# Kernel optimization log

Hardware: AMD Instinct MI355X
Metric: run time of the kernel (lower is better)

The kernel has to match this reference:

```python
import jax, jax.numpy as jnp
import numpy as np

BN_EPS = 1e-6
LN_EPS = 1e-5
ROPE_BASE = 10000.0


def rope(x):
    # x: [..., S, d] ; standard half-split rotary embedding, positions 0..S-1
    S, d = x.shape[-2], x.shape[-1]
    half = d // 2
    inv_freq = 1.0 / (ROPE_BASE ** (jnp.arange(half, dtype=jnp.float32) / half))
    ang = jnp.arange(S, dtype=jnp.float32)[:, None] * inv_freq[None, :]  # [S, half]
    cos, sin = jnp.cos(ang), jnp.sin(ang)
    x1, x2 = x[..., :half], x[..., half:]
    return jnp.concatenate([x1 * cos - x2 * sin, x1 * sin + x2 * cos], axis=-1)


def layernorm(x, g, b):
    m = jnp.mean(x, axis=-1, keepdims=True)
    v = jnp.mean((x - m) ** 2, axis=-1, keepdims=True)
    return (x - m) * jax.lax.rsqrt(v + LN_EPS) * g + b


def rms_batchnorm(x, g, b, running):
    # eval-mode RMSBatchNorm1D: normalize by running RMS^2 buffer
    return x * jax.lax.rsqrt(running + BN_EPS) * g + b


def setup_inputs() -> dict:
    B, S, C, H, QD, KD, VD = 4, 2048, 1536, 8, 128, 128, 192
    key = jax.random.key(0)
    ks = jax.random.split(key, 8)
    sc = 0.02
    return {
        'x': jax.random.normal(ks[0], (B, S, C), dtype=jnp.float32),
        'rms_g': jnp.ones((C,), jnp.float32),
        'rms_b': jnp.zeros((C,), jnp.float32),
        'rms_r': jnp.ones((C,), jnp.float32),
        'Wq': jax.random.normal(ks[1], (H * QD, C), jnp.float32) * sc,
        'Wk': jax.random.normal(ks[2], (KD, C), jnp.float32) * sc,
        'Wv': jax.random.normal(ks[3], (VD, C), jnp.float32) * sc,
        'q_g': jnp.ones((QD,), jnp.float32), 'q_b': jnp.zeros((QD,), jnp.float32),
        'k_g': jnp.ones((KD,), jnp.float32), 'k_b': jnp.zeros((KD,), jnp.float32),
        'v_g': jnp.ones((VD,), jnp.float32), 'v_b': jnp.zeros((VD,), jnp.float32),
        'Wo': jax.random.normal(ks[4], (C, H * VD), jnp.float32) * sc,
        'bo': jnp.zeros((C,), jnp.float32),
        'on_g': jnp.ones((C,), jnp.float32),
        'on_b': jnp.zeros((C,), jnp.float32),
        'on_r': jnp.ones((C,), jnp.float32),
    }


def reference(x, rms_g, rms_b, rms_r, Wq, Wk, Wv, q_g, q_b, k_g, k_b, v_g, v_b, Wo, bo, on_g, on_b, on_r):
    B, S, C = x.shape
    H, QD = 8, Wq.shape[0] // 8
    KD, VD = Wk.shape[0], Wv.shape[0]

    xn = rms_batchnorm(x, rms_g, rms_b, rms_r)

    q = (xn @ Wq.T).reshape(B, S, H, QD)       # [B,S,H,QD]
    q = layernorm(q, q_g, q_b)
    k = layernorm(xn @ Wk.T, k_g, k_b)          # [B,S,KD] shared across heads (MQA)
    v = layernorm(xn @ Wv.T, v_g, v_b)          # [B,S,VD]

    # RoPE along sequence dim
    q = rope(jnp.transpose(q, (0, 2, 1, 3)))    # [B,H,S,QD]
    k = rope(k)
    v = rope(v)

    scale = 1.0 / jnp.sqrt(jnp.float32(KD))
    logits = jnp.einsum('bhsc,bSc->bhsS', q, k) * scale   # [B,H,S,S]
    attn = jax.nn.softmax(logits, axis=-1)
    o = jnp.einsum('bhsS,bSc->bshc', attn, v).reshape(B, S, H * VD)

    y = o @ Wo.T + bo                            # [B,S,C]
    y = rms_batchnorm(y, on_g, on_b, on_r)
    # dropout is identity in eval mode
    return y
```

## Files before the change

kernel.cpp:

```cpp
#include <hip/hip_runtime.h>
#include <math.h>

typedef unsigned short u16;
typedef unsigned int   u32;
typedef __attribute__((ext_vector_type(8))) short bf16x8;
typedef __attribute__((ext_vector_type(4))) float f32x4;

#define DEVI static __device__ __forceinline__

constexpr int Bb = 4, Ss = 2048, Cc = 1536, Hh = 8, QD = 128, KD = 128, VD = 192;
constexpr int NTOK = Bb * Ss;
constexpr int NQKV = Hh*QD + KD + VD;
constexpr int NQKV_PAD = 1536;
constexpr float ATTN_SCALE = 0.08838834764831845f;

constexpr size_t OFF_S1  = 0;
constexpr size_t OFF_B1  = OFF_S1 + Cc*4;
constexpr size_t OFF_S2  = OFF_B1 + Cc*4;
constexpr size_t OFF_B2  = OFF_S2 + Cc*4;
constexpr size_t OFF_CT  = 24576;
constexpr size_t OFF_ST  = OFF_CT  + (size_t)Ss*64*4;
constexpr size_t OFF_CTV = OFF_ST  + (size_t)Ss*64*4;
constexpr size_t OFF_STV = OFF_CTV + (size_t)Ss*96*4;
constexpr size_t OFF_WQKV= OFF_STV + (size_t)Ss*96*4;
constexpr size_t OFF_WO  = OFF_WQKV+ (size_t)NQKV_PAD*Cc*2;
constexpr size_t OFF_XN  = OFF_WO  + (size_t)Cc*Cc*2;
constexpr size_t OFF_QKV = OFF_XN  + (size_t)NTOK*Cc*2;
constexpr size_t OFF_Q   = OFF_QKV + (size_t)NTOK*NQKV*2;
constexpr size_t OFF_K   = OFF_Q   + (size_t)NTOK*(Hh*QD)*2;
constexpr size_t OFF_VT  = OFF_K   + (size_t)NTOK*KD*2;

DEVI u16 f2b(float f) {
  union { float f; u32 u; } v; v.f = f;
  u32 r = v.u + 0x7FFFu + ((v.u >> 16) & 1u);
  return (u16)(r >> 16);
}
DEVI float b2f(u16 h) {
  union { u32 u; float f; } v; v.u = ((u32)h) << 16;
  return v.f;
}
DEVI u32 cvtpk(float lo, float hi) {
  u32 r;
  asm("v_cvt_pk_bf16_f32 %0, %1, %2" : "=v"(r) : "v"(lo), "v"(hi));
  return r;
}
DEVI void gload16(const void* g, void* l) {
  __builtin_amdgcn_global_load_lds(g, l, 16, 0, 0);
}
DEVI f32x4 mfma16(bf16x8 a, bf16x8 b, f32x4 c) {
  return __builtin_amdgcn_mfma_f32_16x16x32_bf16(a, b, c, 0, 0, 0);
}
DEVI int swz64(int byte) {
  return byte ^ ((((byte>>7)&1)<<4) | (((byte>>8)&1)<<5));
}

__global__ __launch_bounds__(256) void k_prep_small(
    const float* __restrict__ rms_g, const float* __restrict__ rms_b, const float* __restrict__ rms_r,
    const float* __restrict__ on_g,  const float* __restrict__ on_b,  const float* __restrict__ on_r,
    const float* __restrict__ bo, char* __restrict__ ws)
{
  int i = blockIdx.x * 256 + threadIdx.x;
  float* s1 = (float*)(ws + OFF_S1);
  float* b1 = (float*)(ws + OFF_B1);
  float* s2 = (float*)(ws + OFF_S2);
  float* b2 = (float*)(ws + OFF_B2);
  float* ct = (float*)(ws + OFF_CT);
  float* st = (float*)(ws + OFF_ST);
  float* ctv= (float*)(ws + OFF_CTV);
  float* stv= (float*)(ws + OFF_STV);
  if (i < Cc) {
    float a = rsqrtf(rms_r[i] + 1e-6f) * rms_g[i];
    s1[i] = a; b1[i] = rms_b[i];
    float c = rsqrtf(on_r[i] + 1e-6f) * on_g[i];
    s2[i] = c; b2[i] = bo[i]*c + on_b[i];
  }
  int j = i - Cc;
  if (j >= 0 && j < Ss*64) {
    int s = j >> 6, f = j & 63;
    float invf = expf(-(float)f * (9.210340371976184f / 64.f));
    float ang = (float)s * invf;
    float sn, cs; sincosf(ang, &sn, &cs);
    ct[j] = cs; st[j] = sn;
  }
  int k = j - Ss*64;
  if (k >= 0 && k < Ss*96) {
    int s = k / 96, f = k - s*96;
    float invf = expf(-(float)f * (9.210340371976184f / 96.f));
    float ang = (float)s * invf;
    float sn, cs; sincosf(ang, &sn, &cs);
    ctv[k] = cs; stv[k] = sn;
  }
}

__global__ __launch_bounds__(256) void k_prep_w(
    const float* __restrict__ Wq, const float* __restrict__ Wk, const float* __restrict__ Wv,
    const float* __restrict__ Wo, char* __restrict__ ws)
{
  u16* wqkv = (u16*)(ws + OFF_WQKV);
  u16* wo   = (u16*)(ws + OFF_WO);
  const int total1 = NQKV_PAD * Cc;
  const int total2 = Cc * Cc;
  for (int i = blockIdx.x*256 + threadIdx.x; i < total1 + total2; i += gridDim.x*256) {
    if (i < total1) {
      int r = i / Cc, c = i - r*Cc;
      float v = 0.f;
      if (r < 1024)      v = Wq[(size_t)r*Cc + c];
      else if (r < 1152) v = Wk[(size_t)(r-1024)*Cc + c];
      else if (r < 1344) v = Wv[(size_t)(r-1152)*Cc + c];
      wqkv[i] = f2b(v);
    } else {
      int t2 = i - total1;
      wo[t2] = f2b(Wo[t2]);
    }
  }
}

__global__ __launch_bounds__(256) void k_xn(const float* __restrict__ x, char* __restrict__ ws)
{
  const float* s1 = (const float*)(ws + OFF_S1);
  const float* b1 = (const float*)(ws + OFF_B1);
  u16* xn = (u16*)(ws + OFF_XN);
  int idx = blockIdx.x*256 + threadIdx.x;
  float4 xv = ((const float4*)x)[idx];
  int c = (idx % (Cc/4)) * 4;
  u32 lo = (u32)f2b(xv.x*s1[c]   + b1[c])   | ((u32)f2b(xv.y*s1[c+1] + b1[c+1]) << 16);
  u32 hi = (u32)f2b(xv.z*s1[c+2] + b1[c+2]) | ((u32)f2b(xv.w*s1[c+3] + b1[c+3]) << 16);
  ((uint2*)xn)[idx] = make_uint2(lo, hi);
}

template <bool EPI>
__global__ __launch_bounds__(512, 2) void k_gemm256(
    const u16* __restrict__ A, const u16* __restrict__ Bw, void* __restrict__ outp,
    int K, int N_store, const float* __restrict__ s2, const float* __restrict__ b2)
{
  __shared__ u16 tiles[4][2][8192];
  const int tid = threadIdx.x;
  const int wid = tid >> 6, l = tid & 63;
  const int lr = l & 15, lh = l >> 4;
  const int wr = wid >> 2, wc = wid & 3;
  const int id  = blockIdx.x + gridDim.x * blockIdx.y;
  const int cpx = (gridDim.x * gridDim.y) >> 3;
  const int sw  = (id & 7) * cpx + (id >> 3);
  const int by  = sw / gridDim.x;
  const int bx  = sw - by * gridDim.x;
  const int m0 = by * 256, n0 = bx * 256;

  const size_t Kb = (size_t)K * 2;
  const char* aBase = (const char*)(A  + (size_t)m0 * K);
  const char* bBase = (const char*)(Bw + (size_t)n0 * K);
  const int o0    = wid*1024 + l*16;
  const int sfl   = swz64(o0);
  const size_t srowb = (size_t)(sfl >> 6) * Kb;
  const int scolb = sfl & 63;
  int aoff[8], boff[4];
#pragma unroll
  for (int mi = 0; mi < 8; mi++) aoff[mi] = swz64((wr*128 + mi*16 + lr)*64 + lh*16);
#pragma unroll
  for (int ni = 0; ni < 4; ni++) boff[ni] = swz64((wc*64  + ni*16 + lr)*64 + lh*16);

  f32x4 acc[8][4] = {};
  const int NT = K >> 5;

#define STAGE(t) {                                                        \
    char* la_ = (char*)tiles[(t) & 3][0] + wid*1024;                      \
    char* lb_ = (char*)tiles[(t) & 3][1] + wid*1024;                      \
    const char* ga_ = aBase + srowb + (size_t)(t)*64 + scolb;             \
    const char* gb_ = bBase + srowb + (size_t)(t)*64 + scolb;             \
    gload16(ga_,            la_);                                         \
    gload16(ga_ + 128*Kb,   la_ + 8192);                                  \
    gload16(gb_,            lb_);                                         \
    gload16(gb_ + 128*Kb,   lb_ + 8192);                                  \
  }

  STAGE(0); STAGE(1); STAGE(2);
  for (int t = 0; t < NT; ++t) {
    if (t + 3 < NT) STAGE(t + 3);
    asm volatile("s_waitcnt vmcnt(12)" ::: "memory");
    __builtin_amdgcn_s_barrier();
    const char* la = (const char*)tiles[t & 3][0];
    const char* lb = (const char*)tiles[t & 3][1];
    bf16x8 af[8], bfr[4];
#pragma unroll
    for (int mi = 0; mi < 8; mi++) af[mi]  = *(const bf16x8*)(la + aoff[mi]);
#pragma unroll
    for (int ni = 0; ni < 4; ni++) bfr[ni] = *(const bf16x8*)(lb + boff[ni]);
    __builtin_amdgcn_s_setprio(1);
#pragma unroll
    for (int mi = 0; mi < 8; mi++)
#pragma unroll
      for (int ni = 0; ni < 4; ni++)
        acc[mi][ni] = mfma16(af[mi], bfr[ni], acc[mi][ni]);
    __builtin_amdgcn_s_setprio(0);
    asm volatile("s_waitcnt lgkmcnt(0)" ::: "memory");
    __builtin_amdgcn_s_barrier();
  }
#undef STAGE

  const int r0 = m0 + wr*128 + lh*4;
  const int c0 = n0 + wc*64 + lr;
#pragma unroll
  for (int mi = 0; mi < 8; mi++) {
#pragma unroll
    for (int ni = 0; ni < 4; ni++) {
      int col = c0 + ni*16;
      if (col < N_store) {
#pragma unroll
        for (int r = 0; r < 4; r++) {
          size_t o = (size_t)(r0 + mi*16 + r) * N_store + col;
          if (EPI) ((float*)outp)[o] = acc[mi][ni][r] * s2[col] + b2[col];
          else     ((u16*)outp)[o]   = f2b(acc[mi][ni][r]);
        }
      }
    }
  }
}

__global__ __launch_bounds__(256) void k_lnrope_qk(
    char* __restrict__ ws,
    const float* __restrict__ q_g, const float* __restrict__ q_b,
    const float* __restrict__ k_g, const float* __restrict__ k_b)
{
  const u16* qkv = (const u16*)(ws + OFF_QKV);
  u16* qo = (u16*)(ws + OFF_Q);
  u16* ko = (u16*)(ws + OFF_K);
  const float* ct = (const float*)(ws + OFF_CT);
  const float* st = (const float*)(ws + OFF_ST);
  const int w = threadIdx.x >> 6, l = threadIdx.x & 63;
  const int rid = blockIdx.x*4 + w;
  const u16* src; u16* dst; const float* g; const float* bb; float osc; int s;
  if (rid < NTOK*Hh) {
    int t = rid >> 3, h = rid & 7;
    s = t & (Ss-1); int b = t >> 11;
    src = qkv + (size_t)t*NQKV + h*QD;
    dst = qo + ((size_t)(b*Hh + h)*Ss + s)*QD;
    g = q_g; bb = q_b; osc = ATTN_SCALE;
  } else {
    int t = rid - NTOK*Hh;
    s = t & (Ss-1);
    src = qkv + (size_t)t*NQKV + Hh*QD;
    dst = ko + (size_t)t*KD;
    g = k_g; bb = k_b; osc = 1.f;
  }
  u32 pk = *(const u32*)(src + 2*l);
  float x0 = b2f((u16)(pk & 0xFFFFu)), x1 = b2f((u16)(pk >> 16));
  float sm = x0 + x1, sq = x0*x0 + x1*x1;
#pragma unroll
  for (int off = 1; off < 64; off <<= 1) { sm += __shfl_xor(sm, off); sq += __shfl_xor(sq, off); }
  float mean = sm * (1.f/128.f);
  float var  = sq * (1.f/128.f) - mean*mean;
  float rstd = rsqrtf(var + 1e-5f);
  int d0 = 2*l;
  float y0 = (x0 - mean)*rstd*g[d0]   + bb[d0];
  float y1 = (x1 - mean)*rstd*g[d0+1] + bb[d0+1];
  float z0 = __shfl_xor(y0, 32);
  float z1 = __shfl_xor(y1, 32);
  int f0 = 2*(l & 31);
  float c0 = ct[s*64 + f0],     s0 = st[s*64 + f0];
  float c1 = ct[s*64 + f0 + 1], s1 = st[s*64 + f0 + 1];
  float o0, o1;
  if (l < 32) { o0 = y0*c0 - z0*s0; o1 = y1*c1 - z1*s1; }
  else        { o0 = z0*s0 + y0*c0; o1 = z1*s1 + y1*c1; }
  o0 *= osc; o1 *= osc;
  *(u32*)(dst + 2*l) = (u32)f2b(o0) | ((u32)f2b(o1) << 16);
}

__global__ __launch_bounds__(256) void k_lnrope_v(
    char* __restrict__ ws, const float* __restrict__ v_g, const float* __restrict__ v_b)
{
  const u16* qkv = (const u16*)(ws + OFF_QKV);
  u16* vo = (u16*)(ws + OFF_VT);
  const float* ct = (const float*)(ws + OFF_CTV);
  const float* st = (const float*)(ws + OFF_STV);
  __shared__ float buf[4][192];
  const int w = threadIdx.x >> 6, l = threadIdx.x & 63;
  const int t = blockIdx.x*4 + w;
  const int s = t & (Ss-1), b = t >> 11;
  const u16* src = qkv + (size_t)t*NQKV + Hh*QD + KD;
  float xs[3]; float sm = 0.f, sq = 0.f;
#pragma unroll
  for (int i2 = 0; i2 < 3; i2++) {
    float xv = b2f(src[l + 64*i2]);
    xs[i2] = xv; buf[w][l + 64*i2] = xv;
    sm += xv; sq += xv*xv;
  }
  __threadfence_block();
#pragma unroll
  for (int off = 1; off < 64; off <<= 1) { sm += __shfl_xor(sm, off); sq += __shfl_xor(sq, off); }
  float mean = sm * (1.f/192.f);
  float var  = sq * (1.f/192.f) - mean*mean;
  float rstd = rsqrtf(var + 1e-5f);
#pragma unroll
  for (int i2 = 0; i2 < 3; i2++) {
    int e = l + 64*i2;
    float val;
    if (e < 96) {
      float x1 = xs[i2], x2 = buf[w][e+96];
      float x1n = (x1-mean)*rstd*v_g[e]    + v_b[e];
      float x2n = (x2-mean)*rstd*v_g[e+96] + v_b[e+96];
      float cs = ct[s*96 + e], sn = st[s*96 + e];
      val = x1n*cs - x2n*sn;
    } else {
      int f = e - 96;
      float x2 = xs[i2], x1 = buf[w][f];
      float x1n = (x1-mean)*rstd*v_g[f] + v_b[f];
      float x2n = (x2-mean)*rstd*v_g[e] + v_b[e];
      float cs = ct[s*96 + f], sn = st[s*96 + f];
      val = x1n*sn + x2n*cs;
    }
    vo[((size_t)b*VD + e)*Ss + s] = f2b(val);
  }
}

__global__ __launch_bounds__(256, 2) void k_attn(const char* __restrict__ ws, u16* __restrict__ O)
{
  const u16* qs = (const u16*)(ws + OFF_Q);
  const u16* ks = (const u16*)(ws + OFF_K);
  const u16* vt = (const u16*)(ws + OFF_VT);
  __shared__ u16 k_lds[64*128];
  __shared__ u16 v_lds[192*64];
  __shared__ u16 p_lds[4][32][64];
  const int tid = threadIdx.x, w = tid >> 6, l = tid & 63;
  const int lr = l & 15, lh = l >> 4;
  const int bid0 = blockIdx.x;
  const int sw = (bid0 & 7)*64 + (bid0 >> 3);
  const int qt = sw & 15, h = (sw >> 4) & 7, b = sw >> 7;
  const int q0 = qt*128 + w*32;
  bf16x8 aq[2][4];
  const u16* qbase = qs + ((size_t)(b*Hh + h)*Ss + q0 + lr)*QD + lh*8;
#pragma unroll
  for (int h2 = 0; h2 < 2; h2++)
#pragma unroll
    for (int kk = 0; kk < 4; kk++)
      aq[h2][kk] = *(const bf16x8*)(qbase + (size_t)h2*16*QD + kk*32);
  float m[2] = {-INFINITY, -INFINITY}, sume[2] = {0.f, 0.f};
  f32x4 acc[2][12] = {};
  const char* ksrc0 = (const char*)(ks + (size_t)b*Ss*KD);
  const char* vsrc0 = (const char*)(vt + (size_t)b*VD*Ss);
  for (int kv0 = 0; kv0 < Ss; kv0 += 64) {
    {
      const char* ksrc = ksrc0 + (size_t)kv0*KD*2;
#pragma unroll
      for (int r = 0; r < 4; r++) {
        int o = r*4096 + w*1024 + l*16;
        gload16(ksrc + (o ^ (((o>>8)&7)<<4)), (char*)k_lds + r*4096 + w*1024);
      }
#pragma unroll
      for (int r = 0; r < 6; r++) {
        int o = r*4096 + w*1024 + l*16;
        int vd = o >> 7, c = o & 127;
        gload16(vsrc0 + (size_t)vd*(Ss*2) + kv0*2 + (c ^ ((vd&7)<<4)),
                (char*)v_lds + r*4096 + w*1024);
      }
    }
    __syncthreads();
    f32x4 sv[2][4] = {};
#pragma unroll
    for (int nt = 0; nt < 4; nt++) {
#pragma unroll
      for (int kk = 0; kk < 4; kk++) {
        int kb = ((nt*16 + lr) << 8) + kk*64 + lh*16;
        kb ^= (lr & 7) << 4;
        bf16x8 bk = *(const bf16x8*)((const char*)k_lds + kb);
        sv[0][nt] = mfma16(bk, aq[0][kk], sv[0][nt]);
        sv[1][nt] = mfma16(bk, aq[1][kk], sv[1][nt]);
      }
    }
#pragma unroll
    for (int h2 = 0; h2 < 2; h2++) {
      float tmx = -INFINITY;
#pragma unroll
      for (int nt = 0; nt < 4; nt++)
        tmx = fmaxf(tmx, fmaxf(fmaxf(sv[h2][nt][0], sv[h2][nt][1]),
                               fmaxf(sv[h2][nt][2], sv[h2][nt][3])));
      tmx = fmaxf(tmx, __shfl_xor(tmx, 16));
      tmx = fmaxf(tmx, __shfl_xor(tmx, 32));
      if (!__all(tmx - m[h2] <= 8.f)) {
        float mnew = fmaxf(m[h2], tmx);
        float scl = __expf(m[h2] - mnew);
        m[h2] = mnew; sume[h2] *= scl;
#pragma unroll
        for (int n = 0; n < 12; n++) acc[h2][n] *= scl;
      }
      float tsum = 0.f;
#pragma unroll
      for (int nt = 0; nt < 4; nt++) {
#pragma unroll
        for (int r2 = 0; r2 < 4; r2++) {
          float e = __expf(sv[h2][nt][r2] - m[h2]);
          sv[h2][nt][r2] = e; tsum += e;
        }
      }
      tsum += __shfl_xor(tsum, 16);
      tsum += __shfl_xor(tsum, 32);
      sume[h2] += tsum;
      {
        char* pw = (char*)&p_lds[w][h2*16 + lr][0];
#pragma unroll
        for (int nt = 0; nt < 4; nt++) {
          u32 w0 = cvtpk(sv[h2][nt][0], sv[h2][nt][1]);
          u32 w1 = cvtpk(sv[h2][nt][2], sv[h2][nt][3]);
          int pcol = (nt*32 + lh*8) ^ ((lr & 7) << 4);
          *(u32*)(pw + pcol)     = w0;
          *(u32*)(pw + pcol + 4) = w1;
        }
      }
    }
    asm volatile("s_waitcnt lgkmcnt(0)" ::: "memory");
    __builtin_amdgcn_sched_barrier(0);
#pragma unroll
    for (int kk2 = 0; kk2 < 2; kk2++) {
      int rcol = (kk2*64 + lh*16) ^ ((lr & 7) << 4);
      bf16x8 pb0 = *(const bf16x8*)((const char*)&p_lds[w][lr][0]      + rcol);
      bf16x8 pb1 = *(const bf16x8*)((const char*)&p_lds[w][16 + lr][0] + rcol);
#pragma unroll
      for (int n = 0; n < 12; n++) {
        int vb = ((n*16 + lr) << 7) + kk2*64 + lh*16;
        vb ^= (lr & 7) << 4;
        bf16x8 av = *(const bf16x8*)((const char*)v_lds + vb);
        acc[0][n] = mfma16(av, pb0, acc[0][n]);
        acc[1][n] = mfma16(av, pb1, acc[1][n]);
      }
    }
    __syncthreads();
  }
#pragma unroll
  for (int h2 = 0; h2 < 2; h2++) {
    float inv = 1.f / sume[h2];
#pragma unroll
    for (int n = 0; n < 12; n++) {
      u32 w0 = cvtpk(acc[h2][n][0]*inv, acc[h2][n][1]*inv);
      u32 w1 = cvtpk(acc[h2][n][2]*inv, acc[h2][n][3]*inv);
      size_t o = ((size_t)b*Ss + q0 + h2*16 + lr)*Cc + h*VD + n*16 + lh*4;
      *(uint2*)(O + o) = make_uint2(w0, w1);
    }
  }
}

extern "C" void kernel_launch(void* const* d_in, const int* in_sizes, int n_in,
                              void* d_out, int out_size, void* d_ws, size_t ws_size,
                              hipStream_t stream)
{
  const float* x     = (const float*)d_in[0];
  const float* rms_g = (const float*)d_in[1];
  const float* rms_b = (const float*)d_in[2];
  const float* rms_r = (const float*)d_in[3];
  const float* Wq    = (const float*)d_in[4];
  const float* Wk    = (const float*)d_in[5];
  const float* Wv    = (const float*)d_in[6];
  const float* q_g   = (const float*)d_in[7];
  const float* q_b   = (const float*)d_in[8];
  const float* k_g   = (const float*)d_in[9];
  const float* k_b   = (const float*)d_in[10];
  const float* v_g   = (const float*)d_in[11];
  const float* v_b   = (const float*)d_in[12];
  const float* Wo    = (const float*)d_in[13];
  const float* bo    = (const float*)d_in[14];
  const float* on_g  = (const float*)d_in[15];
  const float* on_b  = (const float*)d_in[16];
  const float* on_r  = (const float*)d_in[17];
  char* ws = (char*)d_ws;

  k_prep_small<<<dim3((Cc + Ss*64 + Ss*96) / 256), 256, 0, stream>>>(
      rms_g, rms_b, rms_r, on_g, on_b, on_r, bo, ws);
  k_prep_w<<<dim3(2048), 256, 0, stream>>>(Wq, Wk, Wv, Wo, ws);
  k_xn<<<dim3(NTOK*Cc/4/256), 256, 0, stream>>>(x, ws);
  k_gemm256<false><<<dim3(NQKV_PAD/256, NTOK/256), 512, 0, stream>>>(
      (const u16*)(ws + OFF_XN), (const u16*)(ws + OFF_WQKV), (void*)(ws + OFF_QKV),
      Cc, NQKV, nullptr, nullptr);
  k_lnrope_qk<<<dim3((NTOK*Hh + NTOK)/4), 256, 0, stream>>>(ws, q_g, q_b, k_g, k_b);
  k_lnrope_v<<<dim3(NTOK/4), 256, 0, stream>>>(ws, v_g, v_b);
  k_attn<<<dim3(Bb*Hh*(Ss/128)), 256, 0, stream>>>(ws, (u16*)(ws + OFF_XN));
  k_gemm256<true><<<dim3(Cc/256, NTOK/256), 512, 0, stream>>>(
      (const u16*)(ws + OFF_XN), (const u16*)(ws + OFF_WO), d_out,
      Cc, Cc, (const float*)(ws + OFF_S2), (const float*)(ws + OFF_B2));
}
```

Before: 374.1 us.

## Restructure GEMM into double-buffered K=64 tiles with interleaved load/MFMA quadrants

The 256x256 GEMM moves from a 4-stage K=32 pipeline to a 2-stage K=64 double buffer. Each iteration is split into four MFMA quadrants, with the next tile's global-to-LDS loads and the fragment reads spread between them, and the LDS swizzle is changed to an XOR on the row index. The aim is better overlap of memory and matrix work and fewer waits per K step, at the cost of more barriers and a hardcoded K=Cc. The weight-conversion kernel is also vectorised to float4 loads with packed bf16 stores.

```diff
diff --git a/kernel.cpp b/kernel.cpp
--- a/kernel.cpp
+++ b/kernel.cpp
@@ -50,9 +50,6 @@
 DEVI f32x4 mfma16(bf16x8 a, bf16x8 b, f32x4 c) {
   return __builtin_amdgcn_mfma_f32_16x16x32_bf16(a, b, c, 0, 0, 0);
 }
-DEVI int swz64(int byte) {
-  return byte ^ ((((byte>>7)&1)<<4) | (((byte>>8)&1)<<5));
-}
 
 __global__ __launch_bounds__(256) void k_prep_small(
     const float* __restrict__ rms_g, const float* __restrict__ rms_b, const float* __restrict__ rms_r,
@@ -98,20 +95,25 @@
 {
   u16* wqkv = (u16*)(ws + OFF_WQKV);
   u16* wo   = (u16*)(ws + OFF_WO);
-  const int total1 = NQKV_PAD * Cc;
-  const int total2 = Cc * Cc;
+  const int total1 = NQKV_PAD * Cc / 4;
+  const int total2 = Cc * Cc / 4;
   for (int i = blockIdx.x*256 + threadIdx.x; i < total1 + total2; i += gridDim.x*256) {
+    float4 v = make_float4(0.f, 0.f, 0.f, 0.f);
+    u16* dst;
     if (i < total1) {
-      int r = i / Cc, c = i - r*Cc;
-      float v = 0.f;
-      if (r < 1024)      v = Wq[(size_t)r*Cc + c];
-      else if (r < 1152) v = Wk[(size_t)(r-1024)*Cc + c];
-      else if (r < 1344) v = Wv[(size_t)(r-1152)*Cc + c];
-      wqkv[i] = f2b(v);
+      int r = i / 384, c = (i - r*384) * 4;
+      if (r < 1024)      v = *(const float4*)&Wq[(size_t)r*Cc + c];
+      else if (r < 1152) v = *(const float4*)&Wk[(size_t)(r-1024)*Cc + c];
+      else if (r < 1344) v = *(const float4*)&Wv[(size_t)(r-1152)*Cc + c];
+      dst = wqkv + (size_t)i*4;
     } else {
       int t2 = i - total1;
-      wo[t2] = f2b(Wo[t2]);
-    }
+      v = *(const float4*)&Wo[(size_t)t2*4];
+      dst = wo + (size_t)t2*4;
+    }
+    u32 lo = (u32)f2b(v.x) | ((u32)f2b(v.y) << 16);
+    u32 hi = (u32)f2b(v.z) | ((u32)f2b(v.w) << 16);
+    *(uint2*)dst = make_uint2(lo, hi);
   }
 }
 
@@ -129,11 +131,14 @@
 }
 
 template <bool EPI>
-__global__ __launch_bounds__(512, 2) void k_gemm256(
+__global__ __launch_bounds__(512) void k_gemm256(
     const u16* __restrict__ A, const u16* __restrict__ Bw, void* __restrict__ outp,
-    int K, int N_store, const float* __restrict__ s2, const float* __restrict__ b2)
-{
-  __shared__ u16 tiles[4][2][8192];
+    int K_, int N_store, const float* __restrict__ s2, const float* __restrict__ b2)
+{
+  __shared__ u16 tiles[2][2][256*64];
+  constexpr int K = Cc;
+  constexpr int NT = K / 64;
+  constexpr size_t Kb = (size_t)K * 2;
   const int tid = threadIdx.x;
   const int wid = tid >> 6, l = tid & 63;
   const int lr = l & 15, lh = l >> 4;
@@ -145,56 +150,111 @@
   const int bx  = sw - by * gridDim.x;
   const int m0 = by * 256, n0 = bx * 256;
 
-  const size_t Kb = (size_t)K * 2;
-  const char* aBase = (const char*)(A  + (size_t)m0 * K);
-  const char* bBase = (const char*)(Bw + (size_t)n0 * K);
-  const int o0    = wid*1024 + l*16;
-  const int sfl   = swz64(o0);
-  const size_t srowb = (size_t)(sfl >> 6) * Kb;
-  const int scolb = sfl & 63;
-  int aoff[8], boff[4];
-#pragma unroll
-  for (int mi = 0; mi < 8; mi++) aoff[mi] = swz64((wr*128 + mi*16 + lr)*64 + lh*16);
-#pragma unroll
-  for (int ni = 0; ni < 4; ni++) boff[ni] = swz64((wc*64  + ni*16 + lr)*64 + lh*16);
+  const int tid8 = tid >> 3;
+  const int csrc = (((tid & 7) ^ (tid8 & 7)) << 4);
+  const char* aS = (const char*)A  + (size_t)(m0 + tid8) * Kb + csrc;
+  const char* bS = (const char*)Bw + (size_t)(n0 + tid8) * Kb + csrc;
+  char* ldsW = (char*)&tiles[0][0][0] + wid*1024;
+
+#define STAGE2(bf, t, c0_) {                                                   \
+    gload16(((c0_) < 4 ? aS : bS) + (size_t)((c0_)&3)*64*Kb + (size_t)(t)*128, \
+            ldsW + (bf)*65536 + ((c0_) < 4 ? 0 : 32768) + ((c0_)&3)*8192);     \
+    gload16((((c0_)+1) < 4 ? aS : bS) + (size_t)(((c0_)+1)&3)*64*Kb + (size_t)(t)*128, \
+            ldsW + (bf)*65536 + (((c0_)+1) < 4 ? 0 : 32768) + (((c0_)+1)&3)*8192); }
+
+  const int swz = (lr & 7) << 4;
+  int baseA[2], baseB[2];
+#pragma unroll
+  for (int ks = 0; ks < 2; ks++) {
+    baseA[ks] = (((wr*128 + lr) * 128) + ks*64 + lh*16) ^ swz;
+    baseB[ks] = (((wc*64  + lr) * 128) + ks*64 + lh*16) ^ swz;
+  }
 
   f32x4 acc[8][4] = {};
-  const int NT = K >> 5;
-
-#define STAGE(t) {                                                        \
-    char* la_ = (char*)tiles[(t) & 3][0] + wid*1024;                      \
-    char* lb_ = (char*)tiles[(t) & 3][1] + wid*1024;                      \
-    const char* ga_ = aBase + srowb + (size_t)(t)*64 + scolb;             \
-    const char* gb_ = bBase + srowb + (size_t)(t)*64 + scolb;             \
-    gload16(ga_,            la_);                                         \
-    gload16(ga_ + 128*Kb,   la_ + 8192);                                  \
-    gload16(gb_,            lb_);                                         \
-    gload16(gb_ + 128*Kb,   lb_ + 8192);                                  \
-  }
-
-  STAGE(0); STAGE(1); STAGE(2);
+  bf16x8 fa[4][2], fb0[2][2], fb1[2][2];
+
+  STAGE2(0, 0, 0); STAGE2(0, 0, 2); STAGE2(0, 0, 4); STAGE2(0, 0, 6);
+
+#pragma unroll 1
   for (int t = 0; t < NT; ++t) {
-    if (t + 3 < NT) STAGE(t + 3);
-    asm volatile("s_waitcnt vmcnt(12)" ::: "memory");
-    __builtin_amdgcn_s_barrier();
-    const char* la = (const char*)tiles[t & 3][0];
-    const char* lb = (const char*)tiles[t & 3][1];
-    bf16x8 af[8], bfr[4];
-#pragma unroll
-    for (int mi = 0; mi < 8; mi++) af[mi]  = *(const bf16x8*)(la + aoff[mi]);
-#pragma unroll
-    for (int ni = 0; ni < 4; ni++) bfr[ni] = *(const bf16x8*)(lb + boff[ni]);
+    const int buf = t & 1, nbuf = buf ^ 1;
+    const char* la = (const char*)&tiles[buf][0][0];
+    const char* lb = (const char*)&tiles[buf][1][0];
+    if (t + 1 < NT) {
+      STAGE2(nbuf, t+1, 0);
+      asm volatile("s_waitcnt vmcnt(2)" ::: "memory");
+    } else {
+      asm volatile("s_waitcnt vmcnt(0)" ::: "memory");
+    }
+    __builtin_amdgcn_s_barrier();
+#pragma unroll
+    for (int mi = 0; mi < 4; mi++)
+#pragma unroll
+      for (int ks = 0; ks < 2; ks++)
+        fa[mi][ks] = *(const bf16x8*)(la + baseA[ks] + mi*2048);
+#pragma unroll
+    for (int ni = 0; ni < 2; ni++)
+#pragma unroll
+      for (int ks = 0; ks < 2; ks++)
+        fb0[ni][ks] = *(const bf16x8*)(lb + baseB[ks] + ni*2048);
     __builtin_amdgcn_s_setprio(1);
 #pragma unroll
-    for (int mi = 0; mi < 8; mi++)
-#pragma unroll
-      for (int ni = 0; ni < 4; ni++)
-        acc[mi][ni] = mfma16(af[mi], bfr[ni], acc[mi][ni]);
+    for (int mi = 0; mi < 4; mi++)
+#pragma unroll
+      for (int ni = 0; ni < 2; ni++)
+#pragma unroll
+        for (int ks = 0; ks < 2; ks++)
+          acc[mi][ni] = mfma16(fa[mi][ks], fb0[ni][ks], acc[mi][ni]);
     __builtin_amdgcn_s_setprio(0);
-    asm volatile("s_waitcnt lgkmcnt(0)" ::: "memory");
-    __builtin_amdgcn_s_barrier();
-  }
-#undef STAGE
+    __builtin_amdgcn_s_barrier();
+#pragma unroll
+    for (int ni = 0; ni < 2; ni++)
+#pragma unroll
+      for (int ks = 0; ks < 2; ks++)
+        fb1[ni][ks] = *(const bf16x8*)(lb + baseB[ks] + (2+ni)*2048);
+    if (t + 1 < NT) STAGE2(nbuf, t+1, 2);
+    __builtin_amdgcn_s_barrier();
+    __builtin_amdgcn_s_setprio(1);
+#pragma unroll
+    for (int mi = 0; mi < 4; mi++)
+#pragma unroll
+      for (int ni = 0; ni < 2; ni++)
+#pragma unroll
+        for (int ks = 0; ks < 2; ks++)
+          acc[mi][2+ni] = mfma16(fa[mi][ks], fb1[ni][ks], acc[mi][2+ni]);
+    __builtin_amdgcn_s_setprio(0);
+    __builtin_amdgcn_s_barrier();
+#pragma unroll
+    for (int mi = 0; mi < 4; mi++)
+#pragma unroll
+      for (int ks = 0; ks < 2; ks++)
+        fa[mi][ks] = *(const bf16x8*)(la + baseA[ks] + (4+mi)*2048);
+    if (t + 1 < NT) STAGE2(nbuf, t+1, 4);
+    __builtin_amdgcn_s_barrier();
+    __builtin_amdgcn_s_setprio(1);
+#pragma unroll
+    for (int mi = 0; mi < 4; mi++)
+#pragma unroll
+      for (int ni = 0; ni < 2; ni++)
+#pragma unroll
+        for (int ks = 0; ks < 2; ks++)
+          acc[4+mi][2+ni] = mfma16(fa[mi][ks], fb1[ni][ks], acc[4+mi][2+ni]);
+    __builtin_amdgcn_s_setprio(0);
+    __builtin_amdgcn_s_barrier();
+    if (t + 1 < NT) STAGE2(nbuf, t+1, 6);
+    __builtin_amdgcn_s_barrier();
+    __builtin_amdgcn_s_setprio(1);
+#pragma unroll
+    for (int mi = 0; mi < 4; mi++)
+#pragma unroll
+      for (int ni = 0; ni < 2; ni++)
+#pragma unroll
+        for (int ks = 0; ks < 2; ks++)
+          acc[4+mi][ni] = mfma16(fa[mi][ks], fb0[ni][ks], acc[4+mi][ni]);
+    __builtin_amdgcn_s_setprio(0);
+    __builtin_amdgcn_s_barrier();
+  }
+#undef STAGE2
 
   const int r0 = m0 + wr*128 + lh*4;
   const int c0 = n0 + wc*64 + lr;
@@ -462,7 +522,7 @@
 
   k_prep_small<<<dim3((Cc + Ss*64 + Ss*96) / 256), 256, 0, stream>>>(
       rms_g, rms_b, rms_r, on_g, on_b, on_r, bo, ws);
-  k_prep_w<<<dim3(2048), 256, 0, stream>>>(Wq, Wk, Wv, Wo, ws);
+  k_prep_w<<<dim3(1536), 256, 0, stream>>>(Wq, Wk, Wv, Wo, ws);
   k_xn<<<dim3(NTOK*Cc/4/256), 256, 0, stream>>>(x, ws);
   k_gemm256<false><<<dim3(NQKV_PAD/256, NTOK/256), 512, 0, stream>>>(
       (const u16*)(ws + OFF_XN), (const u16*)(ws + OFF_WQKV), (void*)(ws + OFF_QKV),
```

After: 357.3 us. -4.5%, faster.
